# Optimization experiments

Hardware: AMD Instinct MI355X
Metric: run time of the kernel (lower is better)

Reference implementation:

```python
import jax, jax.numpy as jnp
import numpy as np

IMG = 100          # IMG_SIZE
NQ = 4             # N_QUBITS
STEP = 2           # sqrt(NQ)
NP_SIDE = IMG // STEP   # 50 patches per side
NPATCH = NP_SIDE * NP_SIDE  # 2500

# Fixed surrogate for tq.RandomLayer(n_ops=8): 6 param rotations + 2 CNOTs
OPS = [("rx", 0), ("ry", 1), ("rz", 2), ("cnot", (0, 1)),
       ("rx", 3), ("cnot", (2, 3)), ("ry", 0), ("rz", 1)]


def _apply_1q(psi, G, w):
    # psi: [N,2,2,2,2] complex, G: [2,2] complex, wire w
    out = jnp.tensordot(G, psi, axes=[[1], [w + 1]])  # new wire axis at 0
    return jnp.moveaxis(out, 0, w + 1)


def _apply_cnot(psi, c, t):
    p0 = jax.lax.index_in_dim(psi, 0, axis=c + 1, keepdims=True)
    p1 = jax.lax.index_in_dim(psi, 1, axis=c + 1, keepdims=True)
    p1 = jnp.flip(p1, axis=t + 1)  # X on target when control=1
    return jnp.concatenate([p0, p1], axis=c + 1)


def _gate(name, t):
    tc = t.astype(jnp.complex64)
    c, s = jnp.cos(tc / 2), jnp.sin(tc / 2)
    if name == "rx":
        return jnp.stack([jnp.stack([c, -1j * s]), jnp.stack([-1j * s, c])])
    if name == "ry":
        return jnp.stack([jnp.stack([c, -s]), jnp.stack([s, c])])
    # rz
    em, ep = jnp.exp(-0.5j * tc), jnp.exp(0.5j * tc)
    z = jnp.zeros_like(em)
    return jnp.stack([jnp.stack([em, z]), jnp.stack([z, ep])])


def _quanv(x, q_params):
    # x: [B,100,100] -> batched 4-qubit statevector sim over all patches
    B = x.shape[0]
    # patch pixel order: [x[c,r], x[c,r+1], x[c+1,r], x[c+1,r+1]]
    p = x.reshape(B, NP_SIDE, STEP, NP_SIDE, STEP)
    p = p.transpose(0, 1, 3, 2, 4).reshape(B * NPATCH, NQ)  # [N,4] angles
    half = 0.5 * p
    a = jnp.stack([jnp.cos(half), jnp.sin(half)], axis=-1)  # [N,4,2] RY|0>
    psi = jnp.einsum("na,nb,nc,nd->nabcd", a[:, 0], a[:, 1], a[:, 2], a[:, 3])
    psi = psi.astype(jnp.complex64)
    pi = 0
    for name, w in OPS:
        if name == "cnot":
            psi = _apply_cnot(psi, w[0], w[1])
        else:
            psi = _apply_1q(psi, _gate(name, q_params[pi]), w)
            pi += 1
    probs = jnp.abs(psi) ** 2  # [N,2,2,2,2] real
    zsign = jnp.array([1.0, -1.0], dtype=probs.dtype)
    exps = []
    for w in range(NQ):
        zb = zsign.reshape((1,) + (1,) * w + (2,) + (1,) * (NQ - 1 - w))
        exps.append((probs * zb).sum(axis=(1, 2, 3, 4)))
    meas = jnp.stack(exps, axis=-1)  # [N,4] PauliZ expvals
    return meas.reshape(B, NPATCH * NQ).astype(jnp.float32)  # [B,10000]


def setup_inputs() -> dict:
    key = jax.random.key(0)
    k1, k2, k3, k4 = jax.random.split(key, 4)
    x = jax.random.uniform(k1, (64, IMG, IMG), dtype=jnp.float32)
    W = jax.random.normal(k2, (2, IMG * IMG), dtype=jnp.float32) * 0.01
    b = jax.random.normal(k3, (2,), dtype=jnp.float32) * 0.01
    q_params = jax.random.uniform(k4, (6,), dtype=jnp.float32) * 2.0 * np.pi
    return {"x": x, "W": W, "b": b, "q_params": q_params}


def reference(x, W, b, q_params):
    feats = jax.lax.stop_gradient(_quanv(x, q_params))  # torch.no_grad() block
    logits = feats @ W.T + b
    return jax.nn.log_softmax(logits, axis=-1)
```

## Files before the change

kernel.cpp:

```cpp
#include <hip/hip_runtime.h>
#include <math.h>

#define IMG      100
#define NPS      50
#define NPATCH   2500
#define NIMG     64
#define CHUNK    256
#define NCHUNK   10


__global__ __launch_bounds__(256) void quanv_dot_kernel(
    const float* __restrict__ x,
    const float* __restrict__ W,
    const float* __restrict__ qp,
    float* __restrict__ acc)
{
    const int b     = blockIdx.x / NCHUNK;
    const int chunk = blockIdx.x % NCHUNK;
    const int p     = chunk * CHUNK + threadIdx.x;

    float t0 = 0.0f, t1 = 0.0f;

    if (p < NPATCH) {
        float gc[6], gs[6];
        #pragma unroll
        for (int k = 0; k < 6; ++k) {
            __sincosf(0.5f * qp[k], &gs[k], &gc[k]);
        }

        const int pi = p / NPS;
        const int pj = p - pi * NPS;
        const float* xb = x + b * (IMG * IMG) + (2 * pi) * IMG + 2 * pj;
        float ang0 = xb[0];
        float ang1 = xb[1];
        float ang2 = xb[IMG];
        float ang3 = xb[IMG + 1];

        float ca[4], sa[4];
        __sincosf(0.5f * ang0, &sa[0], &ca[0]);
        __sincosf(0.5f * ang1, &sa[1], &ca[1]);
        __sincosf(0.5f * ang2, &sa[2], &ca[2]);
        __sincosf(0.5f * ang3, &sa[3], &ca[3]);

        float2 psi[16];
        #pragma unroll
        for (int i = 0; i < 16; ++i) {
            float v = ((i & 8) ? sa[0] : ca[0]) *
                      ((i & 4) ? sa[1] : ca[1]) *
                      ((i & 2) ? sa[2] : ca[2]) *
                      ((i & 1) ? sa[3] : ca[3]);
            psi[i] = make_float2(v, 0.0f);
        }


        #define APPLY_RX(m, c, s)                                              \
            _Pragma("unroll")                                                  \
            for (int i = 0; i < 16; ++i) if (!(i & (m))) {                     \
                int j = i | (m);                                               \
                float2 p0 = psi[i], p1 = psi[j];                               \
                psi[i] = make_float2((c)*p0.x + (s)*p1.y,                      \
                                     (c)*p0.y - (s)*p1.x);                     \
                psi[j] = make_float2((s)*p0.y + (c)*p1.x,                      \
                                    -(s)*p0.x + (c)*p1.y);                     \
            }

        #define APPLY_RY(m, c, s)                                              \
            _Pragma("unroll")                                                  \
            for (int i = 0; i < 16; ++i) if (!(i & (m))) {                     \
                int j = i | (m);                                               \
                float2 p0 = psi[i], p1 = psi[j];                               \
                psi[i] = make_float2((c)*p0.x - (s)*p1.x,                      \
                                     (c)*p0.y - (s)*p1.y);                     \
                psi[j] = make_float2((s)*p0.x + (c)*p1.x,                      \
                                     (s)*p0.y + (c)*p1.y);                     \
            }

        #define APPLY_RZ(m, c, s)                                              \
            _Pragma("unroll")                                                  \
            for (int i = 0; i < 16; ++i) {                                     \
                float2 pp = psi[i];                                            \
                if (i & (m)) {                                                 \
                    psi[i] = make_float2((c)*pp.x - (s)*pp.y,                  \
                                         (c)*pp.y + (s)*pp.x);                 \
                } else {                                                       \
                    psi[i] = make_float2((c)*pp.x + (s)*pp.y,                  \
                                         (c)*pp.y - (s)*pp.x);                 \
                }                                                              \
            }

        #define APPLY_CNOT(mc, mt)                                             \
            _Pragma("unroll")                                                  \
            for (int i = 0; i < 16; ++i) if ((i & (mc)) && !(i & (mt))) {      \
                int j = i | (mt);                                              \
                float2 tmp = psi[i]; psi[i] = psi[j]; psi[j] = tmp;            \
            }

        APPLY_RX(8, gc[0], gs[0]);
        APPLY_RY(4, gc[1], gs[1]);
        APPLY_RZ(2, gc[2], gs[2]);
        APPLY_CNOT(8, 4);
        APPLY_RX(1, gc[3], gs[3]);
        APPLY_CNOT(2, 1);
        APPLY_RY(8, gc[4], gs[4]);
        APPLY_RZ(4, gc[5], gs[5]);

        float e0 = 0.f, e1 = 0.f, e2 = 0.f, e3 = 0.f;
        #pragma unroll
        for (int i = 0; i < 16; ++i) {
            float pr = psi[i].x * psi[i].x + psi[i].y * psi[i].y;
            e0 += (i & 8) ? -pr : pr;
            e1 += (i & 4) ? -pr : pr;
            e2 += (i & 2) ? -pr : pr;
            e3 += (i & 1) ? -pr : pr;
        }

        const float4 w0 = reinterpret_cast<const float4*>(W)[p];
        const float4 w1 = reinterpret_cast<const float4*>(W)[NPATCH + p];
        t0 = e0 * w0.x + e1 * w0.y + e2 * w0.z + e3 * w0.w;
        t1 = e0 * w1.x + e1 * w1.y + e2 * w1.z + e3 * w1.w;
    }

    #pragma unroll
    for (int off = 32; off > 0; off >>= 1) {
        t0 += __shfl_down(t0, off);
        t1 += __shfl_down(t1, off);
    }
    __shared__ float red0[4], red1[4];
    const int lane = threadIdx.x & 63;
    const int wv   = threadIdx.x >> 6;
    if (lane == 0) { red0[wv] = t0; red1[wv] = t1; }
    __syncthreads();
    if (threadIdx.x == 0) {
        float a0 = red0[0] + red0[1] + red0[2] + red0[3];
        float a1 = red1[0] + red1[1] + red1[2] + red1[3];
        atomicAdd(&acc[b * 2 + 0], a0);
        atomicAdd(&acc[b * 2 + 1], a1);
    }
}

__global__ __launch_bounds__(64) void logsoftmax_kernel(
    const float* __restrict__ acc,
    const float* __restrict__ bias,
    float* __restrict__ out)
{
    const int b = threadIdx.x;
    if (b < NIMG) {
        float l0 = acc[2 * b + 0] + bias[0];
        float l1 = acc[2 * b + 1] + bias[1];
        float m  = fmaxf(l0, l1);
        float lse = m + logf(__expf(l0 - m) + __expf(l1 - m));
        out[2 * b + 0] = l0 - lse;
        out[2 * b + 1] = l1 - lse;
    }
}

extern "C" void kernel_launch(void* const* d_in, const int* in_sizes, int n_in,
                              void* d_out, int out_size, void* d_ws, size_t ws_size,
                              hipStream_t stream) {
    const float* x    = (const float*)d_in[0];
    const float* W    = (const float*)d_in[1];
    const float* bias = (const float*)d_in[2];
    const float* qp   = (const float*)d_in[3];
    float* out = (float*)d_out;
    float* acc = (float*)d_ws;

    hipMemsetAsync(acc, 0, NIMG * 2 * sizeof(float), stream);
    quanv_dot_kernel<<<NIMG * NCHUNK, CHUNK, 0, stream>>>(x, W, qp, acc);
    logsoftmax_kernel<<<1, 64, 0, stream>>>(acc, bias, out);
}
```

Baseline: 68.82 us.

## Fuse quanv, reduction and log-softmax into one kernel per image

Launches one 1024-thread block per image; each thread loops over patches, and the block reduces in shared memory and then applies bias and log-softmax directly. This drops the memset, the atomics and the second kernel launch. In exchange, only 64 blocks run on a GPU with many more compute units, so much of the device may sit idle.

After: 66.10 us. 4.0% less time.

```diff
diff --git a/kernel.cpp b/kernel.cpp
--- a/kernel.cpp
+++ b/kernel.cpp
@@ -5,29 +5,27 @@
 #define NPS      50
 #define NPATCH   2500
 #define NIMG     64
-#define CHUNK    256
-#define NCHUNK   10
+#define BLK      1024
 
 
-__global__ __launch_bounds__(256) void quanv_dot_kernel(
+__global__ __launch_bounds__(BLK) void quanv_fused_kernel(
     const float* __restrict__ x,
     const float* __restrict__ W,
+    const float* __restrict__ bias,
     const float* __restrict__ qp,
-    float* __restrict__ acc)
+    float* __restrict__ out)
 {
-    const int b     = blockIdx.x / NCHUNK;
-    const int chunk = blockIdx.x % NCHUNK;
-    const int p     = chunk * CHUNK + threadIdx.x;
+    const int b = blockIdx.x;
+
+    float gc[6], gs[6];
+    #pragma unroll
+    for (int k = 0; k < 6; ++k) {
+        __sincosf(0.5f * qp[k], &gs[k], &gc[k]);
+    }
 
     float t0 = 0.0f, t1 = 0.0f;
 
-    if (p < NPATCH) {
-        float gc[6], gs[6];
-        #pragma unroll
-        for (int k = 0; k < 6; ++k) {
-            __sincosf(0.5f * qp[k], &gs[k], &gc[k]);
-        }
-
+    for (int p = threadIdx.x; p < NPATCH; p += BLK) {
         const int pi = p / NPS;
         const int pj = p - pi * NPS;
         const float* xb = x + b * (IMG * IMG) + (2 * pi) * IMG + 2 * pj;
@@ -51,7 +49,6 @@
                       ((i & 1) ? sa[3] : ca[3]);
             psi[i] = make_float2(v, 0.0f);
         }
-
 
         #define APPLY_RX(m, c, s)                                              \
             _Pragma("unroll")                                                  \
@@ -116,8 +113,8 @@
 
         const float4 w0 = reinterpret_cast<const float4*>(W)[p];
         const float4 w1 = reinterpret_cast<const float4*>(W)[NPATCH + p];
-        t0 = e0 * w0.x + e1 * w0.y + e2 * w0.z + e3 * w0.w;
-        t1 = e0 * w1.x + e1 * w1.y + e2 * w1.z + e3 * w1.w;
+        t0 += e0 * w0.x + e1 * w0.y + e2 * w0.z + e3 * w0.w;
+        t1 += e0 * w1.x + e1 * w1.y + e2 * w1.z + e3 * w1.w;
     }
 
     #pragma unroll
@@ -125,32 +122,21 @@
         t0 += __shfl_down(t0, off);
         t1 += __shfl_down(t1, off);
     }
-    __shared__ float red0[4], red1[4];
+    __shared__ float red0[BLK / 64], red1[BLK / 64];
     const int lane = threadIdx.x & 63;
     const int wv   = threadIdx.x >> 6;
     if (lane == 0) { red0[wv] = t0; red1[wv] = t1; }
     __syncthreads();
     if (threadIdx.x == 0) {
-        float a0 = red0[0] + red0[1] + red0[2] + red0[3];
-        float a1 = red1[0] + red1[1] + red1[2] + red1[3];
-        atomicAdd(&acc[b * 2 + 0], a0);
-        atomicAdd(&acc[b * 2 + 1], a1);
-    }
-}
-
-__global__ __launch_bounds__(64) void logsoftmax_kernel(
-    const float* __restrict__ acc,
-    const float* __restrict__ bias,
-    float* __restrict__ out)
-{
-    const int b = threadIdx.x;
-    if (b < NIMG) {
-        float l0 = acc[2 * b + 0] + bias[0];
-        float l1 = acc[2 * b + 1] + bias[1];
-        float m  = fmaxf(l0, l1);
+        float l0 = 0.f, l1 = 0.f;
+        #pragma unroll
+        for (int w = 0; w < BLK / 64; ++w) { l0 += red0[w]; l1 += red1[w]; }
+        l0 += bias[0];
+        l1 += bias[1];
+        float m   = fmaxf(l0, l1);
         float lse = m + logf(__expf(l0 - m) + __expf(l1 - m));
-        out[2 * b + 0] = l0 - lse;
-        out[2 * b + 1] = l1 - lse;
+        out[b * 2 + 0] = l0 - lse;
+        out[b * 2 + 1] = l1 - lse;
     }
 }
 
@@ -162,9 +148,6 @@
     const float* bias = (const float*)d_in[2];
     const float* qp   = (const float*)d_in[3];
     float* out = (float*)d_out;
-    float* acc = (float*)d_ws;
 
-    hipMemsetAsync(acc, 0, NIMG * 2 * sizeof(float), stream);
-    quanv_dot_kernel<<<NIMG * NCHUNK, CHUNK, 0, stream>>>(x, W, qp, acc);
-    logsoftmax_kernel<<<1, 64, 0, stream>>>(acc, bias, out);
+    quanv_fused_kernel<<<NIMG, BLK, 0, stream>>>(x, W, bias, qp, out);
 }
```
